# Optimization experiments

Measured on AMD Instinct MI355X. Metric: run time of the kernel, lower is better.

Reference implementation:

```python
import jax, jax.numpy as jnp
import numpy as np

B, H, W = 8, 240, 320
NB = 81  # n_bins + 1 edges
EPS_SILOG = 1e-10
W_SILOG, W_L2, W_BINS = 1.0, 1.0, 1.0  # w_masked = 1.0 -> invalid branch skipped


def _onedirectional_dist(a, b):
    # a: [B, Na], b: [B, Nb] -> per-batch sum over Na of min_k (a_j - b_k)^2
    sq = (a[:, :, None] - b[:, None, :]) ** 2  # [B, Na, Nb] (memory-bound)
    return jnp.min(sq, axis=2).sum(axis=1)  # [B]


def _chamfer(target, bin_edges, mask):
    # mask-aware padding, as in the torch module
    max_target = jnp.max(jnp.where(mask, target, -1e30))
    max_center = jnp.max(bin_edges)
    mx = jnp.maximum(max_target, max_center)
    mn = jnp.minimum(max_target, max_center)
    pad_value = mx + (mx - mn) + 1.0  # eps = 1.0
    nb = bin_edges.shape[0]
    mod_bins = jnp.concatenate([bin_edges, jnp.full((nb, 1), pad_value, bin_edges.dtype)], axis=1)  # [B, NB+1]
    mod_target = jnp.where(mask, target, pad_value).reshape(nb, -1)  # [B, H*W]
    d = _onedirectional_dist(mod_bins, mod_target) + _onedirectional_dist(mod_target, mod_bins)
    return d.mean()


def _masked_mean(x, m):
    cnt = jnp.sum(m.astype(x.dtype))
    return jnp.sum(jnp.where(m, x, 0.0)) / cnt


def _silog(pred, target, mask):
    d = jnp.log(pred + EPS_SILOG) - jnp.log(target + EPS_SILOG)
    m1 = _masked_mean(d, mask)
    m2 = _masked_mean(d * d, mask)
    return 10.0 * jnp.sqrt(m2 - 0.85 * m1 * m1)


def _l2(pred, target, mask):
    return jnp.sqrt(_masked_mean((pred - target) ** 2, mask))


def setup_inputs() -> dict:
    key = jax.random.key(0)
    k1, k2, k3, k4 = jax.random.split(key, 4)
    # positive depth values (log is taken with eps)
    prediction = jax.random.uniform(k1, (B, 1, H, W), jnp.float32, 0.1, 10.0)
    target = jax.random.uniform(k2, (B, 1, H, W), jnp.float32, 0.1, 10.0)
    bin_edges = jax.random.uniform(k3, (B, NB), jnp.float32, 0.1, 10.0)
    mask = jax.random.randint(k4, (B, 1, H, W), 0, 2).astype(bool)
    return {"prediction": prediction, "target": target, "bin_edges": bin_edges, "mask": mask}


def reference(prediction, target, bin_edges, mask):
    chamfer = _chamfer(target, bin_edges, mask)
    silog = _silog(prediction, target, mask)
    l2 = _l2(prediction, target, mask)
    return W_L2 * l2 + W_SILOG * silog + W_BINS * chamfer
```

## Files before the change

### kernel.cpp

```cpp
#include <hip/hip_runtime.h>
#include <math.h>

#define BB   8
#define NB   81
#define HW   76800
#define HW4  19200
#define EPS  1e-10f

#define BPB  19
#define NBLK (BB * BPB)
#define NTHR 1024
#define LUTN 512
#define MAGIC 0x5A5A5A5Au

typedef unsigned long long u64;

#define PT_U 0
#define ST_U 152
#define DA_U 760
#define CA_I 1824
#define CB_I 2480

__device__ __forceinline__ u64 pack(float v) {
    unsigned b = __float_as_uint(v);
    return (u64)b | ((u64)(b ^ MAGIC) << 32);
}
__device__ __forceinline__ float spin_pair(const u64* slot) {
    u64 v;
    for (;;) {
        v = __hip_atomic_load(slot, __ATOMIC_RELAXED, __HIP_MEMORY_SCOPE_AGENT);
        unsigned lo = (unsigned)v, hi = (unsigned)(v >> 32);
        if (__all((lo ^ MAGIC) == hi)) break;
        __builtin_amdgcn_s_sleep(1);
    }
    return __uint_as_float((unsigned)v);
}
__device__ __forceinline__ float lo_f(u64 v) { return __uint_as_float((unsigned)v); }
__device__ __forceinline__ u64 aload64(const u64* p) {
    return __hip_atomic_load(p, __ATOMIC_RELAXED, __HIP_MEMORY_SCOPE_AGENT);
}
__device__ __forceinline__ int aloadi(const int* p) {
    return __hip_atomic_load(p, __ATOMIC_RELAXED, __HIP_MEMORY_SCOPE_AGENT);
}

__device__ __forceinline__ float wsum(float v) {
#pragma unroll
    for (int o = 32; o > 0; o >>= 1) v += __shfl_xor(v, o, 64);
    return v;
}
__device__ __forceinline__ float wmax(float v) {
#pragma unroll
    for (int o = 32; o > 0; o >>= 1) v = fmaxf(v, __shfl_xor(v, o, 64));
    return v;
}
__device__ __forceinline__ float g16sum(float v) {
    v += __shfl_xor(v, 8, 64); v += __shfl_xor(v, 4, 64);
    v += __shfl_xor(v, 2, 64); v += __shfl_xor(v, 1, 64);
    return v;
}
__device__ __forceinline__ float g16max(float v) {
    v = fmaxf(v, __shfl_xor(v, 8, 64)); v = fmaxf(v, __shfl_xor(v, 4, 64));
    v = fmaxf(v, __shfl_xor(v, 2, 64)); v = fmaxf(v, __shfl_xor(v, 1, 64));
    return v;
}

__device__ __forceinline__ int probe_mode(const void* mask, int tid) {
    unsigned pv = ((const unsigned*)mask)[tid & 63];
    bool alli = __all(pv == 0u || pv == 1u);
    bool allf = __all(pv == 0u || pv == 0x3F800000u);
    return alli ? 1 : (allf ? 2 : 0);
}
__device__ __forceinline__ void mask4(const void* mask, int mode, int widx,
                                      int& m0, int& m1, int& m2, int& m3) {
    if (mode == 1)      { uint4  u = ((const uint4*) mask)[widx]; m0 = u.x; m1 = u.y; m2 = u.z; m3 = u.w; }
    else if (mode == 2) { float4 f = ((const float4*)mask)[widx]; m0 = f.x != 0.f; m1 = f.y != 0.f; m2 = f.z != 0.f; m3 = f.w != 0.f; }
    else { unsigned um = ((const unsigned*)mask)[widx];
           m0 = um & 0xFF; m1 = (um >> 8) & 0xFF; m2 = (um >> 16) & 0xFF; m3 = (um >> 24) & 0xFF; }
}

__global__ __launch_bounds__(NTHR, 1) void k_fused(const float* __restrict__ pred,
                                                   const float* __restrict__ tgt,
                                                   const float* __restrict__ bins,
                                                   const void*  __restrict__ mask,
                                                   float* __restrict__ ws,
                                                   float* __restrict__ out) {
    __shared__ float redw[16], redb[16];
    __shared__ float part[16][5];
    __shared__ float sraw[NB], ssrt[NB];
    __shared__ int   lut[LUTN];
    __shared__ int   iA[82], iB[82];
    __shared__ float s_maxB, s_rA, sred[5];
    __shared__ float allb[BB * NB], sbAll[BB * NB];
    __shared__ float fA[BB * 82], fB[BB * 82];
    __shared__ float tmpR[BB][82];
    __shared__ float out8[BB], cntb8[BB];

    int tid = threadIdx.x, bid = blockIdx.x;
    int wid = tid >> 6, lane = tid & 63;
    int b = bid / BPB, c = bid - b * BPB;
    u64* wsu = (u64*)ws;
    int* wsi = (int*)ws;
    int mode = probe_mode(mask, tid);

    const int  idx  = c * NTHR + tid;
    const bool live = (idx < HW4);
    const float4* p4p = (const float4*)(pred + (size_t)b * HW);
    const float4* t4p = (const float4*)(tgt  + (size_t)b * HW);

    float4 t4 = make_float4(0.f, 0.f, 0.f, 0.f);
    float4 p4 = make_float4(0.f, 0.f, 0.f, 0.f);
    int m0 = 0, m1 = 0, m2 = 0, m3 = 0;
    if (live) {
        t4 = t4p[idx];
        p4 = p4p[idx];
        mask4(mask, mode, b * HW4 + idx, m0, m1, m2, m3);
    }

    float mt = 0.f;
    if (m0) mt = fmaxf(mt, t4.x);
    if (m1) mt = fmaxf(mt, t4.y);
    if (m2) mt = fmaxf(mt, t4.z);
    if (m3) mt = fmaxf(mt, t4.w);
    mt = wmax(mt);
    if (lane == 0) redw[wid] = mt;
    float bv = (tid < BB * NB) ? bins[tid] : -INFINITY;
    bv = wmax(bv);
    if (lane == 0) redb[wid] = bv;
    if (tid < NB) sraw[tid] = bins[b * NB + tid];
    __syncthreads();

    if (tid < 16) {
        float v = g16max(redw[tid]);
        if (tid == 0) atomicExch(&wsu[PT_U + bid], pack(v));
    }
    if (tid >= 64 && tid < 80) {
        float v = g16max(redb[tid - 64]);
        if (tid == 64) s_maxB = v;
    }
    if (tid < NB) {
        float v = sraw[tid]; int r = 0;
        for (int k = 0; k < NB; ++k) { float u = sraw[k]; r += (u < v) || (u == v && k < tid); }
        ssrt[r] = v;
    }
    if (tid < 82) { iA[tid] = 0xFF800000; iB[tid] = 0x7F800000; }
    __syncthreads();

    float lo = ssrt[0], hi = ssrt[NB - 1];
    float w = (hi - lo) / (float)LUTN;
    float scale = (hi > lo) ? (float)LUTN / (hi - lo) : 0.f;
    if (tid < LUTN) {
        float edge = lo + (float)tid * w;
        int l = 0, r = NB;
        while (l < r) { int m = (l + r) >> 1; if (ssrt[m] < edge) l = m + 1; else r = m; }
        lut[tid] = l;
    }
    float ptv = -INFINITY;
    if (tid < NBLK) ptv = spin_pair(&wsu[PT_U + tid]);
    ptv = wmax(ptv);
    if (lane == 0) redw[wid] = ptv;
    __syncthreads();

    float maxT = redw[0];
#pragma unroll
    for (int k = 1; k < 16; ++k) maxT = fmaxf(maxT, redw[k]);
    float maxB = s_maxB;
    float mx = fmaxf(maxT, maxB), mn = fminf(maxT, maxB);
    float pad = mx + (mx - mn) + 1.0f;

    float sd = 0.f, sd2 = 0.f, ssq = 0.f, cnt = 0.f, dA = 0.f;
    if (live) {
        float pv_[4] = { p4.x, p4.y, p4.z, p4.w };
        float tv_[4] = { t4.x, t4.y, t4.z, t4.w };
        int   mv_[4] = { m0, m1, m2, m3 };
#pragma unroll
        for (int e = 0; e < 4; ++e) {
            if (!mv_[e]) continue;
            float t = tv_[e], p = pv_[e];
            float d = __logf((p + EPS) / (t + EPS));
            sd += d; sd2 += d * d;
            float er = p - t; ssq += er * er;
            cnt += 1.f;
            int q = (int)((t - lo) * scale);
            q = q < 0 ? 0 : (q > LUTN - 1 ? LUTN - 1 : q);
            int s = lut[q];
            while (s < NB && ssrt[s] <= t) ++s;
            while (s > 0 && ssrt[s - 1] > t) --s;
            float lof = (s > 0)  ? ssrt[s - 1] : -INFINITY;
            float hif = (s < NB) ? ssrt[s]     : pad;
            float dl = t - lof, dh = hif - t;
            dA += fminf(dl * dl, dh * dh);
            int bits = __float_as_int(t);
            atomicMax(&iA[s], bits);
            atomicMin(&iB[s], bits);
        }
    }
    sd = wsum(sd); sd2 = wsum(sd2); ssq = wsum(ssq); cnt = wsum(cnt); dA = wsum(dA);
    if (lane == 0) {
        part[wid][0] = sd; part[wid][1] = sd2; part[wid][2] = ssq;
        part[wid][3] = cnt; part[wid][4] = dA;
    }
    __syncthreads();

    if (tid < 82) {
        int a = iA[tid], bm = iB[tid];
        if (a  != 0xFF800000) atomicMax(&wsi[CA_I + b * 82 + tid], a);
        if (bm != 0x7F800000) atomicMax(&wsi[CB_I + b * 82 + tid], 0x7FFFFFFF - bm);
    }
    if (tid < 64) {
        int q = tid >> 4, r = tid & 15;
        float v = g16sum(part[r][q]);
        if (r == 0) atomicExch(&wsu[ST_U + bid * 4 + q], pack(v));
    }
    if (tid >= 64 && tid < 80) {
        float v = g16sum(part[tid - 64][4]);
        if (tid == 64) s_rA = v;
    }
    asm volatile("s_waitcnt vmcnt(0)" ::: "memory");
    __syncthreads();
    if (tid == 0) atomicExch(&wsu[DA_U + bid], pack(s_rA));

    if (bid != 0) return;

    float dav = 0.f, v0 = 0.f, v1 = 0.f, v2 = 0.f, v3 = 0.f;
    if (tid < NBLK) {
        dav = spin_pair(&wsu[DA_U + tid]);
        v0 = lo_f(aload64(&wsu[ST_U + tid * 4 + 0]));
        v1 = lo_f(aload64(&wsu[ST_U + tid * 4 + 1]));
        v2 = lo_f(aload64(&wsu[ST_U + tid * 4 + 2]));
        v3 = lo_f(aload64(&wsu[ST_U + tid * 4 + 3]));
    }
    v0 = wsum(v0); v1 = wsum(v1); v2 = wsum(v2); v3 = wsum(v3); dav = wsum(dav);
    if (lane == 0) {
        part[wid][0] = v0; part[wid][1] = v1; part[wid][2] = v2;
        part[wid][3] = v3; part[wid][4] = dav;
    }
    if (tid < BB * NB) allb[tid] = bins[tid];
    __syncthreads();
    if (tid < 64) {
        int q = tid >> 4, r = tid & 15;
        float v = g16sum(part[r][q]);
        if (r == 0) sred[q] = v;
    }
    if (tid >= 64 && tid < 80) {
        float v = g16sum(part[tid - 64][4]);
        if (tid == 64) sred[4] = v;
    }
    if (tid < BB) {
        float s = 0.f;
        for (int j = 0; j < BPB; ++j)
            s += lo_f(aload64(&wsu[ST_U + (tid * BPB + j) * 4 + 3]));
        cntb8[tid] = s;
    }
    if (tid < BB * 82) {
        int ea = aloadi(&wsi[CA_I + tid]);
        int eb = aloadi(&wsi[CB_I + tid]);
        fA[tid] = (ea < 0) ? -INFINITY : __int_as_float(ea);
        fB[tid] = (eb < 0) ?  INFINITY : __int_as_float(0x7FFFFFFF - eb);
    }
    __syncthreads();
    if (tid < BB * NB) {
        int b2 = tid / NB, j = tid - b2 * NB;
        float v = allb[tid]; int r = 0;
        for (int k = 0; k < NB; ++k) { float u = allb[b2 * NB + k]; r += (u < v) || (u == v && k < j); }
        sbAll[b2 * NB + r] = v;
    }
    __syncthreads();

    if (tid < BB) {
        const float* SBb = &sbAll[tid * NB];
        bool anyInv = (cntb8[tid] != (float)HW);
        float rmin = anyInv ? pad : INFINITY;
        { float d = rmin - pad; tmpR[tid][81] = d * d; }
        for (int k = NB - 1; k >= 0; --k) {
            rmin = fminf(rmin, fB[tid * 82 + k + 1]);
            float d = rmin - SBb[k];
            tmpR[tid][k] = d * d;
        }
        float lmax = -INFINITY, sb = 0.f;
        for (int k = 0; k <= NB; ++k) {
            lmax = fmaxf(lmax, fA[tid * 82 + k]);
            float sk = (k < NB) ? SBb[k] : pad;
            float d = sk - lmax;
            sb += fminf(d * d, tmpR[tid][k]);
        }
        out8[tid] = sb;
    }
    __syncthreads();

    if (tid == 0) {
        float s0 = sred[0], s1 = sred[1], s2 = sred[2], s3 = sred[3], sa = sred[4];
        float sumB = 0.f;
        for (int i = 0; i < BB; ++i) sumB += out8[i];
        float m1 = s0 / s3, m2 = s1 / s3;
        float silog = 10.0f * sqrtf(fmaxf(m2 - 0.85f * m1 * m1, 0.0f));
        float l2 = sqrtf(s2 / s3);
        float chamfer = (sa + sumB) / (float)BB;
        out[0] = l2 + silog + chamfer;
    }
}

extern "C" void kernel_launch(void* const* d_in, const int* in_sizes, int n_in,
                              void* d_out, int out_size, void* d_ws, size_t ws_size,
                              hipStream_t stream) {
    (void)in_sizes; (void)n_in; (void)out_size; (void)ws_size;
    const float* pred = (const float*)d_in[0];
    const float* tgt  = (const float*)d_in[1];
    const float* bins = (const float*)d_in[2];
    const void*  mask = d_in[3];
    float* ws  = (float*)d_ws;
    float* out = (float*)d_out;

    k_fused<<<NBLK, NTHR, 0, stream>>>(pred, tgt, bins, mask, ws, out);
}
```

Measured before the change: 23.44 us.

## Hoist silog/L2 stats before grid barrier and let last-arriving block finalize

Moves the per-element log/L2/count accumulation ahead of the grid-wide max-target spin-wait, so this arithmetic overlaps the wait for other blocks and its partials are published early. The final reduction is no longer pinned to block 0 spinning on all others. Each block checks whether every block's slot is already valid and returns if not, so whichever block sees all slots filled does the final combine. This removes the tail spin in block 0 but adds an extra barrier and a global scan per block. If no block, or more than one, sees a complete set, the output could be missing or written twice.

```diff
diff --git a/kernel.cpp b/kernel.cpp
--- a/kernel.cpp
+++ b/kernel.cpp
@@ -25,12 +25,14 @@
     unsigned b = __float_as_uint(v);
     return (u64)b | ((u64)(b ^ MAGIC) << 32);
 }
+__device__ __forceinline__ bool pair_ok(u64 v) {
+    return (((unsigned)v) ^ MAGIC) == (unsigned)(v >> 32);
+}
 __device__ __forceinline__ float spin_pair(const u64* slot) {
     u64 v;
     for (;;) {
         v = __hip_atomic_load(slot, __ATOMIC_RELAXED, __HIP_MEMORY_SCOPE_AGENT);
-        unsigned lo = (unsigned)v, hi = (unsigned)(v >> 32);
-        if (__all((lo ^ MAGIC) == hi)) break;
+        if (__all(pair_ok(v))) break;
         __builtin_amdgcn_s_sleep(1);
     }
     return __uint_as_float((unsigned)v);
@@ -89,11 +91,11 @@
     __shared__ float sraw[NB], ssrt[NB];
     __shared__ int   lut[LUTN];
     __shared__ int   iA[82], iB[82];
-    __shared__ float s_maxB, s_rA, sred[5];
+    __shared__ float s_maxB, s_rA;
     __shared__ float allb[BB * NB], sbAll[BB * NB];
     __shared__ float fA[BB * 82], fB[BB * 82];
     __shared__ float tmpR[BB][82];
-    __shared__ float out8[BB], cntb8[BB];
+    __shared__ float out8[BB], cntb8[BB], sred[5];
 
     int tid = threadIdx.x, bid = blockIdx.x;
     int wid = tid >> 6, lane = tid & 63;
@@ -116,26 +118,43 @@
         mask4(mask, mode, b * HW4 + idx, m0, m1, m2, m3);
     }
 
-    float mt = 0.f;
-    if (m0) mt = fmaxf(mt, t4.x);
-    if (m1) mt = fmaxf(mt, t4.y);
-    if (m2) mt = fmaxf(mt, t4.z);
-    if (m3) mt = fmaxf(mt, t4.w);
-    mt = wmax(mt);
-    if (lane == 0) redw[wid] = mt;
+    float sd = 0.f, sd2 = 0.f, ssq = 0.f, cnt = 0.f, mt = 0.f;
+    {
+        float pv_[4] = { p4.x, p4.y, p4.z, p4.w };
+        float tv_[4] = { t4.x, t4.y, t4.z, t4.w };
+        int   mv_[4] = { m0, m1, m2, m3 };
+#pragma unroll
+        for (int e = 0; e < 4; ++e) {
+            if (!mv_[e]) continue;
+            float t = tv_[e], p = pv_[e];
+            float d = __logf((p + EPS) / (t + EPS));
+            sd += d; sd2 += d * d;
+            float er = p - t; ssq += er * er;
+            cnt += 1.f;
+            mt = fmaxf(mt, t);
+        }
+    }
+    sd = wsum(sd); sd2 = wsum(sd2); ssq = wsum(ssq); cnt = wsum(cnt); mt = wmax(mt);
+    if (lane == 0) {
+        part[wid][0] = sd; part[wid][1] = sd2; part[wid][2] = ssq;
+        part[wid][3] = cnt; part[wid][4] = mt;
+    }
     float bv = (tid < BB * NB) ? bins[tid] : -INFINITY;
     bv = wmax(bv);
     if (lane == 0) redb[wid] = bv;
     if (tid < NB) sraw[tid] = bins[b * NB + tid];
     __syncthreads();
 
-    if (tid < 16) {
-        float v = g16max(redw[tid]);
-        if (tid == 0) atomicExch(&wsu[PT_U + bid], pack(v));
-    }
-    if (tid >= 64 && tid < 80) {
-        float v = g16max(redb[tid - 64]);
-        if (tid == 64) s_maxB = v;
+    if (tid < 64) {
+        int q = tid >> 4, r = tid & 15;
+        float v = g16sum(part[r][q]);
+        if (r == 0) atomicExch(&wsu[ST_U + bid * 4 + q], pack(v));
+    } else if (tid < 80) {
+        float v = g16max(part[tid & 15][4]);
+        if (tid == 64) atomicExch(&wsu[PT_U + bid], pack(v));
+    } else if (tid >= 128 && tid < 144) {
+        float v = g16max(redb[tid & 15]);
+        if (tid == 128) s_maxB = v;
     }
     if (tid < NB) {
         float v = sraw[tid]; int r = 0;
@@ -167,19 +186,14 @@
     float mx = fmaxf(maxT, maxB), mn = fminf(maxT, maxB);
     float pad = mx + (mx - mn) + 1.0f;
 
-    float sd = 0.f, sd2 = 0.f, ssq = 0.f, cnt = 0.f, dA = 0.f;
+    float dA = 0.f;
     if (live) {
-        float pv_[4] = { p4.x, p4.y, p4.z, p4.w };
         float tv_[4] = { t4.x, t4.y, t4.z, t4.w };
         int   mv_[4] = { m0, m1, m2, m3 };
 #pragma unroll
         for (int e = 0; e < 4; ++e) {
             if (!mv_[e]) continue;
-            float t = tv_[e], p = pv_[e];
-            float d = __logf((p + EPS) / (t + EPS));
-            sd += d; sd2 += d * d;
-            float er = p - t; ssq += er * er;
-            cnt += 1.f;
+            float t = tv_[e];
             int q = (int)((t - lo) * scale);
             q = q < 0 ? 0 : (q > LUTN - 1 ? LUTN - 1 : q);
             int s = lut[q];
@@ -194,11 +208,8 @@
             atomicMin(&iB[s], bits);
         }
     }
-    sd = wsum(sd); sd2 = wsum(sd2); ssq = wsum(ssq); cnt = wsum(cnt); dA = wsum(dA);
-    if (lane == 0) {
-        part[wid][0] = sd; part[wid][1] = sd2; part[wid][2] = ssq;
-        part[wid][3] = cnt; part[wid][4] = dA;
-    }
+    dA = wsum(dA);
+    if (lane == 0) part[wid][0] = dA;
     __syncthreads();
 
     if (tid < 82) {
@@ -206,24 +217,26 @@
         if (a  != 0xFF800000) atomicMax(&wsi[CA_I + b * 82 + tid], a);
         if (bm != 0x7F800000) atomicMax(&wsi[CB_I + b * 82 + tid], 0x7FFFFFFF - bm);
     }
-    if (tid < 64) {
-        int q = tid >> 4, r = tid & 15;
-        float v = g16sum(part[r][q]);
-        if (r == 0) atomicExch(&wsu[ST_U + bid * 4 + q], pack(v));
-    }
     if (tid >= 64 && tid < 80) {
-        float v = g16sum(part[tid - 64][4]);
+        float v = g16sum(part[tid & 15][0]);
         if (tid == 64) s_rA = v;
     }
     asm volatile("s_waitcnt vmcnt(0)" ::: "memory");
     __syncthreads();
     if (tid == 0) atomicExch(&wsu[DA_U + bid], pack(s_rA));
-
-    if (bid != 0) return;
+    asm volatile("s_waitcnt vmcnt(0)" ::: "memory");
+    __syncthreads();
+
+    bool ok = true;
+    if (tid < NBLK) ok = pair_ok(aload64(&wsu[DA_U + tid]));
+    ok = __all(ok);
+    if (lane == 0) redw[wid] = ok ? 1.f : 0.f;
+    __syncthreads();
+    if (!(redw[0] > 0.f && redw[1] > 0.f && redw[2] > 0.f)) return;
 
     float dav = 0.f, v0 = 0.f, v1 = 0.f, v2 = 0.f, v3 = 0.f;
     if (tid < NBLK) {
-        dav = spin_pair(&wsu[DA_U + tid]);
+        dav = lo_f(aload64(&wsu[DA_U + tid]));
         v0 = lo_f(aload64(&wsu[ST_U + tid * 4 + 0]));
         v1 = lo_f(aload64(&wsu[ST_U + tid * 4 + 1]));
         v2 = lo_f(aload64(&wsu[ST_U + tid * 4 + 2]));
@@ -240,9 +253,8 @@
         int q = tid >> 4, r = tid & 15;
         float v = g16sum(part[r][q]);
         if (r == 0) sred[q] = v;
-    }
-    if (tid >= 64 && tid < 80) {
-        float v = g16sum(part[tid - 64][4]);
+    } else if (tid < 80) {
+        float v = g16sum(part[tid & 15][4]);
         if (tid == 64) sred[4] = v;
     }
     if (tid < BB) {
```

Measured after the change: 25.79 us. 10.1% more time.
